# Kernel optimization log

Hardware: AMD Instinct MI355X
Metric: run time of the kernel (lower is better)

The kernel has to match this reference:

```python
import jax, jax.numpy as jnp
import numpy as np

IN_C, OUT_C, K, STRIDE, PAD, N_EXPERTS = 64, 128, 3, 1, 1, 4
B, H, W = 32, 64, 64


def setup_inputs() -> dict:
    key = jax.random.key(0)
    k1, k2, k3, k4 = jax.random.split(key, 4)
    x = jax.random.normal(k1, (B, IN_C, H, W), dtype=jnp.float32)
    idx = jax.random.randint(k2, (B,), 0, N_EXPERTS, dtype=jnp.int64)
    # Expert conv weights/biases (PyTorch Conv2d layout: [out_c, in_c, kh, kw])
    fan_in = IN_C * K * K
    bound = 1.0 / np.sqrt(fan_in)
    Wc = jax.random.uniform(k3, (N_EXPERTS, OUT_C, IN_C, K, K), dtype=jnp.float32,
                            minval=-bound, maxval=bound)
    bc = jax.random.uniform(k4, (N_EXPERTS, OUT_C), dtype=jnp.float32,
                            minval=-bound, maxval=bound)
    return {"x": x, "idx": idx, "Wc": Wc, "bc": bc}


def _conv2d(x, w, b):
    # x: [B, C_in, H, W], w: [C_out, C_in, K, K], b: [C_out]
    y = jax.lax.conv_general_dilated(
        x, w,
        window_strides=(STRIDE, STRIDE),
        padding=[(PAD, PAD), (PAD, PAD)],
        dimension_numbers=("NCHW", "OIHW", "NCHW"),
    )
    return y + b[None, :, None, None]


def reference(x, idx, Wc, bc):
    # Compute every expert's conv for every sample (faithful to the torch code),
    # then gather each sample's selected expert output.
    results = jax.vmap(lambda w, b: _conv2d(x, w, b))(Wc, bc)  # [E, B, C_out, H, W]
    results = jnp.moveaxis(results, 0, 1)                      # [B, E, C_out, H, W]
    out = jnp.take_along_axis(
        results, idx[:, None, None, None, None].astype(jnp.int32), axis=1
    )  # [B, 1, C_out, H, W]
    return jnp.squeeze(out, axis=1)
```

## Files before the change

### kernel.cpp

```cpp
#include <hip/hip_runtime.h>
#include <hip/hip_bf16.h>


#define IC 64
#define OC 128
#define HH 64
#define WW 64

typedef short short8 __attribute__((ext_vector_type(8)));
typedef float float16 __attribute__((ext_vector_type(16)));

static __device__ __forceinline__ ushort f2bf(float v) {
    __hip_bfloat16 h = __float2bfloat16(v);
    return *(ushort*)&h;
}

__global__ __launch_bounds__(256)
void reorder_w(const float* __restrict__ Wc, ushort* __restrict__ wout) {
    const int tid = blockIdx.x * 256 + threadIdx.x;
    const int ic  = tid & 63;
    const int eoc = tid >> 6;
    const int oc  = eoc & 127;
    const int e   = eoc >> 7;
    const float* src = Wc + (size_t)tid * 9;
    float v[9];
#pragma unroll
    for (int tp = 0; tp < 9; ++tp) v[tp] = src[tp];
#pragma unroll
    for (int tp = 0; tp < 9; ++tp)
        wout[((((size_t)e * 9 + tp) * 8 + (ic >> 3)) * 128 + oc) * 8 + (ic & 7)] = f2bf(v[tp]);
}

__global__ __launch_bounds__(256)
void moe_conv_mfma(const float* __restrict__ x, const int* __restrict__ idx,
                   const ushort* __restrict__ wre, const float* __restrict__ bc,
                   float* __restrict__ out) {
    __shared__ __align__(16) ushort xs[4 * 8 * 66 * 8];
    __shared__ __align__(16) ushort wlds[8192];
    __shared__ float bias[128];

    const int t    = threadIdx.x;
    const int rp   = blockIdx.x;
    const int b    = blockIdx.y;
    const int row0 = rp * 2;
    const int e    = ((unsigned)idx[b]) & 3;

    if (t < 128) {
        const int r = t >> 5, ich = (t >> 2) & 7, side = (t >> 1) & 1, q = t & 1;
        const int hc = side ? 65 : 0;
        ushort4 z = {0, 0, 0, 0};
        *(ushort4*)&xs[(((r * 8 + ich) * 66 + hc) * 8 + q * 4)] = z;
    } else {
        bias[t - 128] = bc[e * 128 + (t - 128)];
    }

    const float* xb = x + (size_t)b * IC * HH * WW;
    {
        const int gc   = t & 63;
        const int csel = t >> 6;
        for (int it = 0; it < 16; ++it) {
            const int combo = it * 4 + csel;
            const int r = combo >> 4, ich = (combo >> 1) & 7, q = combo & 1;
            const int gr = row0 - 1 + r;
            ushort4 u = {0, 0, 0, 0};
            if ((unsigned)gr < (unsigned)HH) {
                const int ic0 = ich * 8 + q * 4;
                u.x = f2bf(xb[((ic0 + 0) * HH + gr) * WW + gc]);
                u.y = f2bf(xb[((ic0 + 1) * HH + gr) * WW + gc]);
                u.z = f2bf(xb[((ic0 + 2) * HH + gr) * WW + gc]);
                u.w = f2bf(xb[((ic0 + 3) * HH + gr) * WW + gc]);
            }
            *(ushort4*)&xs[(((r * 8 + ich) * 66 + (gc + 1)) * 8 + q * 4)] = u;
        }
    }

    const int l      = t & 63;
    const int lane31 = l & 31;
    const int lhi    = l >> 5;
    const int wv     = t >> 6;
    const int w0     = wv & 1;
    const int pr     = wv >> 1;

    float16 acc[2][2];
#pragma unroll
    for (int a = 0; a < 2; ++a)
#pragma unroll
        for (int cg = 0; cg < 2; ++cg)
#pragma unroll
            for (int r = 0; r < 16; ++r) acc[a][cg][r] = 0.0f;

    const ushort* wsrc = wre + (size_t)e * 9 * 8192;

    for (int tap = 0; tap < 9; ++tap) {
        __syncthreads();
        {
            const ushort* g0 = wsrc + tap * 8192;
#pragma unroll
            for (int i = 0; i < 4; ++i) {
                const int g = i * 256 + t;
                __builtin_amdgcn_global_load_lds(
                    (const __attribute__((address_space(1))) unsigned int*)(g0 + g * 8),
                    (__attribute__((address_space(3))) unsigned int*)&wlds[g * 8],
                    16, 0, 0);
            }
        }
        __syncthreads();

        const int kh = tap / 3;
        const int kw = tap - kh * 3;
        const int rbase  = (pr + kh) * 8;
        const int hbase0 = lane31 + kw;

#pragma unroll
        for (int ks = 0; ks < 4; ++ks) {
            const int ich = ks * 2 + lhi;
            const short8 a0 = *(const short8*)&wlds[(ich * 128 + w0 * 64 + lane31) * 8];
            const short8 a1 = *(const short8*)&wlds[(ich * 128 + w0 * 64 + 32 + lane31) * 8];
            const short8 b0 = *(const short8*)&xs[((rbase + ich) * 66 + hbase0) * 8];
            const short8 b1 = *(const short8*)&xs[((rbase + ich) * 66 + hbase0 + 32) * 8];
            acc[0][0] = __builtin_amdgcn_mfma_f32_32x32x16_bf16(a0, b0, acc[0][0], 0, 0, 0);
            acc[0][1] = __builtin_amdgcn_mfma_f32_32x32x16_bf16(a0, b1, acc[0][1], 0, 0, 0);
            acc[1][0] = __builtin_amdgcn_mfma_f32_32x32x16_bf16(a1, b0, acc[1][0], 0, 0, 0);
            acc[1][1] = __builtin_amdgcn_mfma_f32_32x32x16_bf16(a1, b1, acc[1][1], 0, 0, 0);
        }
    }

#pragma unroll
    for (int a = 0; a < 2; ++a) {
        const int ocb = w0 * 64 + a * 32 + 4 * lhi;
#pragma unroll
        for (int reg = 0; reg < 16; ++reg) {
            const int oc = ocb + (reg & 3) + 8 * (reg >> 2);
            const float bv = bias[oc];
            const size_t base = (((size_t)b * OC + oc) * HH + (row0 + pr)) * WW;
            out[base + lane31]      = acc[a][0][reg] + bv;
            out[base + 32 + lane31] = acc[a][1][reg] + bv;
        }
    }
}

extern "C" void kernel_launch(void* const* d_in, const int* in_sizes, int n_in,
                              void* d_out, int out_size, void* d_ws, size_t ws_size,
                              hipStream_t stream) {
    const float* x   = (const float*)d_in[0];
    const int*   idx = (const int*)d_in[1];
    const float* Wc  = (const float*)d_in[2];
    const float* bc  = (const float*)d_in[3];
    float* out  = (float*)d_out;
    ushort* wre = (ushort*)d_ws;

    reorder_w<<<128, 256, 0, stream>>>(Wc, wre);
    dim3 grid(32, 32);
    moe_conv_mfma<<<grid, 256, 0, stream>>>(x, idx, wre, bc, out);
}
```

Before: 124.9 us.

## Process four output rows per block with 512 threads to amortize weight staging

The conv kernel now computes four output rows per block using 8 waves instead of two rows with 4 waves. Each weight tap loaded into LDS is reused across twice as many rows, and the input halo overhead drops from 4 staged rows per 2 outputs to 6 per 4. The weight-reorder kernel is also restructured so each block handles one expert/tap, writing coalesced ushort2 outputs at the cost of strided reads. Fewer blocks (512) may reduce occupancy and latency hiding on a large GPU.

```diff
diff --git a/kernel.cpp b/kernel.cpp
--- a/kernel.cpp
+++ b/kernel.cpp
@@ -17,50 +17,58 @@
 
 __global__ __launch_bounds__(256)
 void reorder_w(const float* __restrict__ Wc, ushort* __restrict__ wout) {
-    const int tid = blockIdx.x * 256 + threadIdx.x;
-    const int ic  = tid & 63;
-    const int eoc = tid >> 6;
-    const int oc  = eoc & 127;
-    const int e   = eoc >> 7;
-    const float* src = Wc + (size_t)tid * 9;
-    float v[9];
-#pragma unroll
-    for (int tp = 0; tp < 9; ++tp) v[tp] = src[tp];
-#pragma unroll
-    for (int tp = 0; tp < 9; ++tp)
-        wout[((((size_t)e * 9 + tp) * 8 + (ic >> 3)) * 128 + oc) * 8 + (ic & 7)] = f2bf(v[tp]);
+    const int blk = blockIdx.x;
+    const int e   = blk / 9;
+    const int tap = blk - e * 9;
+    const float* __restrict__ src = Wc + (size_t)e * OC * IC * 9 + tap;
+    ushort2* __restrict__ dst = (ushort2*)(wout + (size_t)blk * 8192);
+    for (int j = threadIdx.x; j < 4096; j += 256) {
+        const int ich = j >> 9;
+        const int oc  = (j >> 2) & 127;
+        const int ip  = j & 3;
+        const int ic  = ich * 8 + ip * 2;
+        const float v0 = src[(oc * IC + ic) * 9];
+        const float v1 = src[(oc * IC + ic + 1) * 9];
+        ushort2 u;
+        u.x = f2bf(v0);
+        u.y = f2bf(v1);
+        dst[j] = u;
+    }
 }
 
-__global__ __launch_bounds__(256)
+__global__ __launch_bounds__(512)
 void moe_conv_mfma(const float* __restrict__ x, const int* __restrict__ idx,
                    const ushort* __restrict__ wre, const float* __restrict__ bc,
                    float* __restrict__ out) {
-    __shared__ __align__(16) ushort xs[4 * 8 * 66 * 8];
+    __shared__ __align__(16) ushort xs[6 * 8 * 66 * 8];
     __shared__ __align__(16) ushort wlds[8192];
     __shared__ float bias[128];
 
     const int t    = threadIdx.x;
-    const int rp   = blockIdx.x;
+    const int rq   = blockIdx.x;
     const int b    = blockIdx.y;
-    const int row0 = rp * 2;
+    const int row0 = rq * 4;
     const int e    = ((unsigned)idx[b]) & 3;
 
-    if (t < 128) {
-        const int r = t >> 5, ich = (t >> 2) & 7, side = (t >> 1) & 1, q = t & 1;
+    if (t < 192) {
+        const int r = t >> 5, rem = t & 31;
+        const int ich = rem >> 2, side = (rem >> 1) & 1, q = rem & 1;
         const int hc = side ? 65 : 0;
         ushort4 z = {0, 0, 0, 0};
         *(ushort4*)&xs[(((r * 8 + ich) * 66 + hc) * 8 + q * 4)] = z;
-    } else {
-        bias[t - 128] = bc[e * 128 + (t - 128)];
+    } else if (t < 320) {
+        bias[t - 192] = bc[e * OC + (t - 192)];
     }
 
     const float* xb = x + (size_t)b * IC * HH * WW;
     {
         const int gc   = t & 63;
         const int csel = t >> 6;
-        for (int it = 0; it < 16; ++it) {
-            const int combo = it * 4 + csel;
-            const int r = combo >> 4, ich = (combo >> 1) & 7, q = combo & 1;
+#pragma unroll
+        for (int it = 0; it < 12; ++it) {
+            const int combo = it * 8 + csel;
+            const int r = combo >> 4, rem = combo & 15;
+            const int ich = rem >> 1, q = rem & 1;
             const int gr = row0 - 1 + r;
             ushort4 u = {0, 0, 0, 0};
             if ((unsigned)gr < (unsigned)HH) {
@@ -74,9 +82,8 @@
         }
     }
 
-    const int l      = t & 63;
-    const int lane31 = l & 31;
-    const int lhi    = l >> 5;
+    const int lane31 = t & 31;
+    const int lhi    = (t >> 5) & 1;
     const int wv     = t >> 6;
     const int w0     = wv & 1;
     const int pr     = wv >> 1;
@@ -96,8 +103,8 @@
         {
             const ushort* g0 = wsrc + tap * 8192;
 #pragma unroll
-            for (int i = 0; i < 4; ++i) {
-                const int g = i * 256 + t;
+            for (int i = 0; i < 2; ++i) {
+                const int g = i * 512 + t;
                 __builtin_amdgcn_global_load_lds(
                     (const __attribute__((address_space(1))) unsigned int*)(g0 + g * 8),
                     (__attribute__((address_space(3))) unsigned int*)&wlds[g * 8],
@@ -108,16 +115,16 @@
 
         const int kh = tap / 3;
         const int kw = tap - kh * 3;
-        const int rbase  = (pr + kh) * 8;
-        const int hbase0 = lane31 + kw;
+        const int rr = pr + kh;
+        const int hb = lane31 + kw;
 
 #pragma unroll
         for (int ks = 0; ks < 4; ++ks) {
             const int ich = ks * 2 + lhi;
             const short8 a0 = *(const short8*)&wlds[(ich * 128 + w0 * 64 + lane31) * 8];
             const short8 a1 = *(const short8*)&wlds[(ich * 128 + w0 * 64 + 32 + lane31) * 8];
-            const short8 b0 = *(const short8*)&xs[((rbase + ich) * 66 + hbase0) * 8];
-            const short8 b1 = *(const short8*)&xs[((rbase + ich) * 66 + hbase0 + 32) * 8];
+            const short8 b0 = *(const short8*)&xs[((rr * 8 + ich) * 66 + hb) * 8];
+            const short8 b1 = *(const short8*)&xs[((rr * 8 + ich) * 66 + hb + 32) * 8];
             acc[0][0] = __builtin_amdgcn_mfma_f32_32x32x16_bf16(a0, b0, acc[0][0], 0, 0, 0);
             acc[0][1] = __builtin_amdgcn_mfma_f32_32x32x16_bf16(a0, b1, acc[0][1], 0, 0, 0);
             acc[1][0] = __builtin_amdgcn_mfma_f32_32x32x16_bf16(a1, b0, acc[1][0], 0, 0, 0);
@@ -149,7 +156,7 @@
     float* out  = (float*)d_out;
     ushort* wre = (ushort*)d_ws;
 
-    reorder_w<<<128, 256, 0, stream>>>(Wc, wre);
-    dim3 grid(32, 32);
-    moe_conv_mfma<<<grid, 256, 0, stream>>>(x, idx, wre, bc, out);
+    reorder_w<<<36, 256, 0, stream>>>(Wc, wre);
+    dim3 grid(16, 32);
+    moe_conv_mfma<<<grid, 512, 0, stream>>>(x, idx, wre, bc, out);
 }
```

Measured after the change: 114.6 us. 1.09x faster.
